# Performance work log

Measured on AMD Instinct MI355X. Metric: run time of the kernel, lower is better.

## Reference

```python
import jax, jax.numpy as jnp
import numpy as np

N_NODES = 100000
N_EDGES = 1600000
D_FEAT = 128


def setup_inputs() -> dict:
    key = jax.random.key(0)
    k1, k2, k3, k4 = jax.random.split(key, 4)
    support = jax.random.normal(k1, (N_NODES, D_FEAT), dtype=jnp.float32)
    vals = jax.random.uniform(k2, (N_EDGES,), dtype=jnp.float32)
    rows = jax.random.randint(k3, (N_EDGES,), 0, N_NODES, dtype=jnp.int64)
    cols = jax.random.randint(k4, (N_EDGES,), 0, N_NODES, dtype=jnp.int64)
    return {"support": support, "vals": vals, "rows": rows, "cols": cols}


def reference(support, vals, rows, cols):
    # out = adj @ support, adj given in COO: adj[rows[e], cols[e]] = vals[e]
    # Gather neighbor features, scale by edge weight, scatter-add to row nodes.
    msgs = vals[:, None] * support[cols]          # [E, F]
    out = jax.ops.segment_sum(msgs, rows, num_segments=support.shape[0])  # [N, F]
    return out
```

## Files before the change

### kernel.cpp

```cpp
#include <hip/hip_runtime.h>
#include <hip/hip_bf16.h>
#include <hip/hip_fp16.h>


#define D_FEAT 128
#define F4 32
#define H4 32
#define STRIDE 64
#define CELL 32
#define OVF_CAP 131072
#define EPT 8
#define MAXIT 8
#define MAXSLOT 8192

typedef float    vfloat4 __attribute__((ext_vector_type(4)));
typedef _Float16 half4v  __attribute__((ext_vector_type(4)));
typedef _Float16 half8v  __attribute__((ext_vector_type(8)));


__global__ __launch_bounds__(1024) void
phase1_bin_kernel(const float4* __restrict__ support4,
                  half8v* __restrict__ supporth,
                  const int* __restrict__ rows,
                  const int* __restrict__ cols,
                  const float* __restrict__ vals,
                  int2* __restrict__ coarse,
                  int* __restrict__ cellcnt,
                  int4* __restrict__ ovf,
                  int* __restrict__ ovf_count,
                  int E, int BT, int NBLK, int ND, int n8) {
    int b = blockIdx.x;
    int tid = threadIdx.x;

    if (b >= NBLK) {
        int m = (b - NBLK) * 1024 + tid;
        if (m < n8) {
            float4 a0 = support4[(size_t)m * 2];
            float4 a1 = support4[(size_t)m * 2 + 1];
            half8v h;
            h[0] = (_Float16)a0.x; h[1] = (_Float16)a0.y;
            h[2] = (_Float16)a0.z; h[3] = (_Float16)a0.w;
            h[4] = (_Float16)a1.x; h[5] = (_Float16)a1.y;
            h[6] = (_Float16)a1.z; h[7] = (_Float16)a1.w;
            supporth[m] = h;
        }
        return;
    }

    __shared__ int hist[512];
    for (int i = tid; i < 512; i += 1024) hist[i] = 0;
    __syncthreads();

    int t = b * 1024 + tid;
    int   r[EPT];
    int   c[EPT];
    float v[EPT];
    int   rk[EPT];

    #pragma unroll
    for (int i = 0; i < EPT; ++i) {
        int e = t + i * BT;
        r[i] = (e < E) ? rows[e] : -1;
    }
    #pragma unroll
    for (int i = 0; i < EPT; ++i) {
        int e = t + i * BT;
        if (e < E) { c[i] = cols[e]; v[i] = vals[e]; }
    }
    #pragma unroll
    for (int i = 0; i < EPT; ++i)
        rk[i] = (r[i] >= 0) ? atomicAdd(&hist[r[i] >> 8], 1) : 0;

    #pragma unroll
    for (int i = 0; i < EPT; ++i) {
        if (r[i] < 0) continue;
        int d = r[i] >> 8;
        if (rk[i] < CELL) {
            int2 q;
            q.x = ((r[i] & 255) << 17) | c[i];
            q.y = __float_as_int(v[i]);
            coarse[((size_t)d * NBLK + b) * CELL + rk[i]] = q;
        } else {
            int o = atomicAdd(ovf_count, 1);
            if (o < OVF_CAP) {
                int4 q;
                q.x = r[i]; q.y = c[i]; q.z = __float_as_int(v[i]); q.w = 0;
                ovf[o] = q;
            }
        }
    }
    __syncthreads();
    for (int d = tid; d < ND; d += 1024) {
        int h = hist[d];
        cellcnt[(size_t)d * NBLK + b] = (h < CELL) ? h : CELL;
    }
}


__global__ __launch_bounds__(1024) void
bucket_csr_gather_kernel(const half4v* __restrict__ supporth,
                         const int2* __restrict__ coarse,
                         const int* __restrict__ cellcnt,
                         float4* __restrict__ out4,
                         int NBLK, int N) {
    __shared__ int  cnt[257];
    __shared__ int  off[257];
    __shared__ int2 csr[MAXSLOT + 8];

    const int d   = blockIdx.x;
    const int tid = threadIdx.x;
    const int2* cbase = coarse  + (size_t)d * NBLK * CELL;
    const int*  ccnt  = cellcnt + (size_t)d * NBLK;
    const int total = NBLK * CELL;

    if (tid < 257) cnt[tid] = 0;
    __syncthreads();

    int2 ent[MAXIT];
    int  err[MAXIT];
    int  ernk[MAXIT];
    #pragma unroll
    for (int it = 0; it < MAXIT; ++it) {
        int s = tid + it * 1024;
        err[it] = -1;
        if (s < total && (s & (CELL - 1)) < ccnt[s >> 5]) {
            int2 q = cbase[s];
            int r = (q.x >> 17) & 255;
            ent[it].x = q.x & 0x1FFFF;
            ent[it].y = q.y;
            err[it] = r;
            ernk[it] = atomicAdd(&cnt[r], 1);
        }
    }
    __syncthreads();

    if (tid < 64) {
        int4 c4 = ((int4*)cnt)[tid];
        int t0 = c4.x;
        int t1 = t0 + c4.y;
        int t2 = t1 + c4.z;
        int t3 = t2 + c4.w;
        int inc = t3;
        #pragma unroll
        for (int dd = 1; dd < 64; dd <<= 1) {
            int t = __shfl_up(inc, dd, 64);
            if (tid >= dd) inc += t;
        }
        int excl = inc - t3;
        off[tid * 4 + 0] = excl;
        off[tid * 4 + 1] = excl + t0;
        off[tid * 4 + 2] = excl + t1;
        off[tid * 4 + 3] = excl + t2;
        if (tid == 63) off[256] = inc;
    }
    __syncthreads();

    #pragma unroll
    for (int it = 0; it < MAXIT; ++it) {
        if (err[it] >= 0)
            csr[off[err[it]] + ernk[it]] = ent[it];
    }
    __syncthreads();

    const int grp = tid >> 5;
    const int j   = tid & 31;
    const int base = d << 8;
    for (int rq = 0; rq < 8; ++rq) {
        int r   = (rq << 5) + grp;
        int beg = off[r];
        int end = off[r + 1];
        float4 acc[4];
        #pragma unroll
        for (int u = 0; u < 4; ++u) acc[u] = {0.f, 0.f, 0.f, 0.f};
        for (int k0 = beg; k0 < end; k0 += 8) {
            int   cc[8];
            float vv[8];
            #pragma unroll
            for (int u = 0; u < 8; ++u) {
                int2 e = csr[k0 + u];
                bool ib = (k0 + u) < end;
                cc[u] = ib ? e.x : 0;
                vv[u] = ib ? __int_as_float(e.y) : 0.f;
            }
            half4v s[8];
            #pragma unroll
            for (int u = 0; u < 8; ++u)
                s[u] = supporth[(size_t)cc[u] * H4 + j];
            #pragma unroll
            for (int u = 0; u < 8; ++u) {
                acc[u & 3].x += vv[u] * (float)s[u][0];
                acc[u & 3].y += vv[u] * (float)s[u][1];
                acc[u & 3].z += vv[u] * (float)s[u][2];
                acc[u & 3].w += vv[u] * (float)s[u][3];
            }
        }
        int row = base + r;
        if (row < N) {
            vfloat4 res;
            res.x = (acc[0].x + acc[1].x) + (acc[2].x + acc[3].x);
            res.y = (acc[0].y + acc[1].y) + (acc[2].y + acc[3].y);
            res.z = (acc[0].z + acc[1].z) + (acc[2].z + acc[3].z);
            res.w = (acc[0].w + acc[1].w) + (acc[2].w + acc[3].w);
            __builtin_nontemporal_store(res, (vfloat4*)&out4[(size_t)row * F4 + j]);
        }
    }
}


__global__ void ovf_scatter_kernel(const float* __restrict__ support,
                                   const int4* __restrict__ ovf,
                                   const int* __restrict__ ovf_count,
                                   float* __restrict__ out, int cap) {
    int gid = blockIdx.x * blockDim.x + threadIdx.x;
    int i = gid >> 5;
    int j = gid & 31;
    int istride = (gridDim.x * blockDim.x) >> 5;
    int cnt = *ovf_count;
    if (cnt > cap) cnt = cap;
    for (; i < cnt; i += istride) {
        int4 q = ovf[i];
        float v = __int_as_float(q.z);
        const float4* s4 = (const float4*)support + (size_t)q.y * F4 + j;
        float4 s = *s4;
        float* o = out + (size_t)q.x * D_FEAT + j * 4;
        unsafeAtomicAdd(o + 0, v * s.x);
        unsafeAtomicAdd(o + 1, v * s.y);
        unsafeAtomicAdd(o + 2, v * s.z);
        unsafeAtomicAdd(o + 3, v * s.w);
    }
}


__global__ void convert_kernel(const float4* __restrict__ in,
                               half8v* __restrict__ out, int n8) {
    int t = blockIdx.x * blockDim.x + threadIdx.x;
    if (t >= n8) return;
    float4 a = in[(size_t)t * 2];
    float4 b = in[(size_t)t * 2 + 1];
    half8v h;
    h[0] = (_Float16)a.x; h[1] = (_Float16)a.y;
    h[2] = (_Float16)a.z; h[3] = (_Float16)a.w;
    h[4] = (_Float16)b.x; h[5] = (_Float16)b.y;
    h[6] = (_Float16)b.z; h[7] = (_Float16)b.w;
    out[t] = h;
}

__global__ void gather_half_kernel(const half4v* __restrict__ supporth,
                                   const int* __restrict__ cursor,
                                   const int2* __restrict__ pairs,
                                   float4* __restrict__ out4, int n_nodes) {
    unsigned int t = blockIdx.x * blockDim.x + threadIdx.x;
    unsigned int row = t >> 5;
    unsigned int j = t & 31;
    if (row >= (unsigned int)n_nodes) return;
    int deg = cursor[row];
    if (deg > STRIDE) deg = STRIDE;
    const int2* pr = pairs + (size_t)row * STRIDE;
    int2 z = {0, 0};
    int2 p0 = ((int)j < deg) ? pr[j] : z;
    int2 p1 = ((int)(j + 32) < deg) ? pr[j + 32] : z;
    int   c0 = p0.x;  float v0 = __int_as_float(p0.y);
    int   c1 = p1.x;  float v1 = __int_as_float(p1.y);
    int degr = (deg + 7) & ~7;
    float4 acc[4];
    #pragma unroll
    for (int u = 0; u < 4; ++u) acc[u] = {0.f, 0.f, 0.f, 0.f};
    for (int k = 0; k < degr; k += 8) {
        int   cc[8];
        float vv[8];
        #pragma unroll
        for (int u = 0; u < 8; ++u) {
            int kk = k + u;
            cc[u] = __shfl(kk < 32 ? c0 : c1, kk & 31, 32);
            vv[u] = __shfl(kk < 32 ? v0 : v1, kk & 31, 32);
        }
        half4v s[8];
        #pragma unroll
        for (int u = 0; u < 8; ++u)
            s[u] = supporth[(size_t)cc[u] * H4 + j];
        #pragma unroll
        for (int u = 0; u < 8; ++u) {
            acc[u & 3].x += vv[u] * (float)s[u][0];
            acc[u & 3].y += vv[u] * (float)s[u][1];
            acc[u & 3].z += vv[u] * (float)s[u][2];
            acc[u & 3].w += vv[u] * (float)s[u][3];
        }
    }
    vfloat4 res;
    res.x = (acc[0].x + acc[1].x) + (acc[2].x + acc[3].x);
    res.y = (acc[0].y + acc[1].y) + (acc[2].y + acc[3].y);
    res.z = (acc[0].z + acc[1].z) + (acc[2].z + acc[3].z);
    res.w = (acc[0].w + acc[1].w) + (acc[2].w + acc[3].w);
    __builtin_nontemporal_store(res, (vfloat4*)&out4[(size_t)row * F4 + j]);
}

__global__ void bucket_ilp_kernel(const int* __restrict__ rows,
                                  const int* __restrict__ cols,
                                  const float* __restrict__ vals,
                                  int* __restrict__ cursor,
                                  int* __restrict__ ovf_count,
                                  int2* __restrict__ pairs,
                                  int4* __restrict__ ovf,
                                  int n_edges, int gstride) {
    int tid = blockIdx.x * blockDim.x + threadIdx.x;
    int   r[EPT];
    int   c[EPT];
    float v[EPT];
    int   slot[EPT];
    #pragma unroll
    for (int i = 0; i < EPT; ++i) {
        int e = tid + i * gstride;
        r[i] = (e < n_edges) ? rows[e] : -1;
    }
    #pragma unroll
    for (int i = 0; i < EPT; ++i) {
        int e = tid + i * gstride;
        if (e < n_edges) { c[i] = cols[e]; v[i] = vals[e]; }
    }
    #pragma unroll
    for (int i = 0; i < EPT; ++i)
        slot[i] = (r[i] >= 0) ? atomicAdd(&cursor[r[i]], 1) : 0;
    #pragma unroll
    for (int i = 0; i < EPT; ++i) {
        if (r[i] < 0) continue;
        int2 p;
        p.x = c[i];
        p.y = __float_as_int(v[i]);
        if (slot[i] < STRIDE) {
            pairs[(size_t)r[i] * STRIDE + slot[i]] = p;
        } else {
            int o = atomicAdd(ovf_count, 1);
            if (o < OVF_CAP) {
                int4 q; q.x = r[i]; q.y = p.x; q.z = p.y; q.w = 0;
                ovf[o] = q;
            }
        }
    }
}


__global__ void gc_scatter_kernel(const float* __restrict__ support,
                                  const float* __restrict__ vals,
                                  const int* __restrict__ rows,
                                  const int* __restrict__ cols,
                                  float* __restrict__ out, int n_edges) {
    unsigned int t = blockIdx.x * blockDim.x + threadIdx.x;
    unsigned int e = t >> 5;
    unsigned int j = t & 31;
    if (e >= (unsigned int)n_edges) return;
    int r = rows[e];
    int c = cols[e];
    float v = vals[e];
    const float4* s4 = reinterpret_cast<const float4*>(support) + (size_t)c * F4 + j;
    float4 s = *s4;
    float* o = out + (size_t)r * D_FEAT + j * 4;
    unsafeAtomicAdd(o + 0, v * s.x);
    unsafeAtomicAdd(o + 1, v * s.y);
    unsafeAtomicAdd(o + 2, v * s.z);
    unsafeAtomicAdd(o + 3, v * s.w);
}


extern "C" void kernel_launch(void* const* d_in, const int* in_sizes, int n_in,
                              void* d_out, int out_size, void* d_ws, size_t ws_size,
                              hipStream_t stream) {
    const float* support = (const float*)d_in[0];
    const float* vals    = (const float*)d_in[1];
    const int*   rows    = (const int*)d_in[2];
    const int*   cols    = (const int*)d_in[3];
    float* out = (float*)d_out;

    int E = in_sizes[1];
    int N = in_sizes[0] / D_FEAT;
    int n8 = N * D_FEAT / 8;
    int ND = (N + 255) >> 8;
    int NBLK = (E + 1024 * EPT - 1) / (1024 * EPT);
    int BT = NBLK * 1024;

    char* ws = (char*)d_ws;
    size_t cur = 0;
    auto carve = [&](size_t bytes) -> void* {
        void* p = ws + cur;
        cur += (bytes + 255) & ~(size_t)255;
        return p;
    };

    {
        size_t save = cur;
        int2*   coarse    = (int2*)carve((size_t)ND * NBLK * CELL * 8);
        int*    cellcnt   = (int*)carve((size_t)ND * NBLK * 4);
        int4*   ovf       = (int4*)carve((size_t)OVF_CAP * 16);
        int*    ovf_count = (int*)carve(256);
        half8v* supporth  = (half8v*)carve((size_t)N * D_FEAT * 2);
        if (cur <= ws_size && ND <= 512 && NBLK * CELL <= MAXSLOT) {
            (void)hipMemsetAsync(ovf_count, 0, 4, stream);
            int cblocks = (n8 + 1023) / 1024;
            phase1_bin_kernel<<<NBLK + cblocks, 1024, 0, stream>>>(
                (const float4*)support, supporth, rows, cols, vals,
                coarse, cellcnt, ovf, ovf_count, E, BT, NBLK, ND, n8);
            bucket_csr_gather_kernel<<<ND, 1024, 0, stream>>>(
                (const half4v*)supporth, coarse, cellcnt, (float4*)out, NBLK, N);
            ovf_scatter_kernel<<<512, 256, 0, stream>>>(
                support, ovf, ovf_count, out, OVF_CAP);
            return;
        }
        cur = save;
    }

    {
        size_t save = cur;
        int*    cursor   = (int*)carve((size_t)(N + 1) * 4);
        int2*   pairs    = (int2*)carve((size_t)N * STRIDE * 8);
        int4*   ovf      = (int4*)carve((size_t)8192 * 16);
        half8v* supporth = (half8v*)carve((size_t)N * D_FEAT * 2);
        if (cur <= ws_size) {
            int* ovf_count = cursor + N;
            int bthreads = (E + EPT - 1) / EPT;
            int bblocks = (bthreads + 255) / 256;
            int gstride = bblocks * 256;
            (void)hipMemsetAsync(cursor, 0, (size_t)(N + 1) * 4, stream);
            convert_kernel<<<(n8 + 255) / 256, 256, 0, stream>>>(
                (const float4*)support, supporth, n8);
            bucket_ilp_kernel<<<bblocks, 256, 0, stream>>>(
                rows, cols, vals, cursor, ovf_count, pairs, ovf, E, gstride);
            unsigned int gthreads = (unsigned int)N * 32;
            gather_half_kernel<<<(gthreads + 255) / 256, 256, 0, stream>>>(
                (const half4v*)supporth, cursor, pairs, (float4*)out, N);
            ovf_scatter_kernel<<<512, 256, 0, stream>>>(
                support, ovf, ovf_count, out, 8192);
            return;
        }
        cur = save;
    }

    (void)hipMemsetAsync(d_out, 0, (size_t)out_size * sizeof(float), stream);
    unsigned int total = (unsigned int)E * 32;
    gc_scatter_kernel<<<(total + 255) / 256, 256, 0, stream>>>(
        support, vals, rows, cols, out, E);
}
```

Before: 202.2 us.

## Use 16-byte half8 gathers in bucket kernel and split conversion into separate kernel

In the gather phase, 16 lanes per row each load a half8 vector of 16 bytes instead of 32 lanes loading half4, so one row's feature vector takes fewer, wider load instructions, and each block now handles 64 rows per pass instead of 32. Each thread keeps two split accumulators of eight floats and issues two float4 stores. The fp32-to-fp16 conversion of support is moved out of the binning kernel into its own launch of 256-thread blocks. That adds a kernel launch and serializes conversion after binning, where the two previously ran together in one grid.

New measurement: 211.2 us. 1.04x slower.

```diff
diff --git a/kernel.cpp b/kernel.cpp
--- a/kernel.cpp
+++ b/kernel.cpp
@@ -6,6 +6,7 @@
 #define D_FEAT 128
 #define F4 32
 #define H4 32
+#define H8 16
 #define STRIDE 64
 #define CELL 32
 #define OVF_CAP 131072
@@ -19,33 +20,16 @@
 
 
 __global__ __launch_bounds__(1024) void
-phase1_bin_kernel(const float4* __restrict__ support4,
-                  half8v* __restrict__ supporth,
-                  const int* __restrict__ rows,
-                  const int* __restrict__ cols,
-                  const float* __restrict__ vals,
-                  int2* __restrict__ coarse,
-                  int* __restrict__ cellcnt,
-                  int4* __restrict__ ovf,
-                  int* __restrict__ ovf_count,
-                  int E, int BT, int NBLK, int ND, int n8) {
+bin_kernel(const int* __restrict__ rows,
+           const int* __restrict__ cols,
+           const float* __restrict__ vals,
+           int2* __restrict__ coarse,
+           int* __restrict__ cellcnt,
+           int4* __restrict__ ovf,
+           int* __restrict__ ovf_count,
+           int E, int BT, int NBLK, int ND) {
     int b = blockIdx.x;
     int tid = threadIdx.x;
-
-    if (b >= NBLK) {
-        int m = (b - NBLK) * 1024 + tid;
-        if (m < n8) {
-            float4 a0 = support4[(size_t)m * 2];
-            float4 a1 = support4[(size_t)m * 2 + 1];
-            half8v h;
-            h[0] = (_Float16)a0.x; h[1] = (_Float16)a0.y;
-            h[2] = (_Float16)a0.z; h[3] = (_Float16)a0.w;
-            h[4] = (_Float16)a1.x; h[5] = (_Float16)a1.y;
-            h[6] = (_Float16)a1.z; h[7] = (_Float16)a1.w;
-            supporth[m] = h;
-        }
-        return;
-    }
 
     __shared__ int hist[512];
     for (int i = tid; i < 512; i += 1024) hist[i] = 0;
@@ -97,8 +81,23 @@
 }
 
 
+__global__ void convert_kernel(const float4* __restrict__ in,
+                               half8v* __restrict__ out, int n8) {
+    int t = blockIdx.x * blockDim.x + threadIdx.x;
+    if (t >= n8) return;
+    float4 a = in[(size_t)t * 2];
+    float4 b = in[(size_t)t * 2 + 1];
+    half8v h;
+    h[0] = (_Float16)a.x; h[1] = (_Float16)a.y;
+    h[2] = (_Float16)a.z; h[3] = (_Float16)a.w;
+    h[4] = (_Float16)b.x; h[5] = (_Float16)b.y;
+    h[6] = (_Float16)b.z; h[7] = (_Float16)b.w;
+    out[t] = h;
+}
+
+
 __global__ __launch_bounds__(1024) void
-bucket_csr_gather_kernel(const half4v* __restrict__ supporth,
+bucket_csr_gather_kernel(const half8v* __restrict__ supporth,
                          const int2* __restrict__ coarse,
                          const int* __restrict__ cellcnt,
                          float4* __restrict__ out4,
@@ -162,16 +161,15 @@
     }
     __syncthreads();
 
-    const int grp = tid >> 5;
-    const int j   = tid & 31;
+    const int g = tid >> 4;
+    const int i = tid & 15;
     const int base = d << 8;
-    for (int rq = 0; rq < 8; ++rq) {
-        int r   = (rq << 5) + grp;
+    for (int rq = 0; rq < 4; ++rq) {
+        int r   = (rq << 6) + g;
         int beg = off[r];
         int end = off[r + 1];
-        float4 acc[4];
-        #pragma unroll
-        for (int u = 0; u < 4; ++u) acc[u] = {0.f, 0.f, 0.f, 0.f};
+        vfloat4 a00 = {0.f,0.f,0.f,0.f}, a01 = {0.f,0.f,0.f,0.f};
+        vfloat4 a10 = {0.f,0.f,0.f,0.f}, a11 = {0.f,0.f,0.f,0.f};
         for (int k0 = beg; k0 < end; k0 += 8) {
             int   cc[8];
             float vv[8];
@@ -182,26 +180,44 @@
                 cc[u] = ib ? e.x : 0;
                 vv[u] = ib ? __int_as_float(e.y) : 0.f;
             }
-            half4v s[8];
+            half8v s[8];
             #pragma unroll
             for (int u = 0; u < 8; ++u)
-                s[u] = supporth[(size_t)cc[u] * H4 + j];
+                s[u] = supporth[(size_t)cc[u] * H8 + i];
             #pragma unroll
             for (int u = 0; u < 8; ++u) {
-                acc[u & 3].x += vv[u] * (float)s[u][0];
-                acc[u & 3].y += vv[u] * (float)s[u][1];
-                acc[u & 3].z += vv[u] * (float)s[u][2];
-                acc[u & 3].w += vv[u] * (float)s[u][3];
+                float v = vv[u];
+                if (u & 1) {
+                    a10.x += v * (float)s[u][0];
+                    a10.y += v * (float)s[u][1];
+                    a10.z += v * (float)s[u][2];
+                    a10.w += v * (float)s[u][3];
+                    a11.x += v * (float)s[u][4];
+                    a11.y += v * (float)s[u][5];
+                    a11.z += v * (float)s[u][6];
+                    a11.w += v * (float)s[u][7];
+                } else {
+                    a00.x += v * (float)s[u][0];
+                    a00.y += v * (float)s[u][1];
+                    a00.z += v * (float)s[u][2];
+                    a00.w += v * (float)s[u][3];
+                    a01.x += v * (float)s[u][4];
+                    a01.y += v * (float)s[u][5];
+                    a01.z += v * (float)s[u][6];
+                    a01.w += v * (float)s[u][7];
+                }
             }
         }
         int row = base + r;
         if (row < N) {
-            vfloat4 res;
-            res.x = (acc[0].x + acc[1].x) + (acc[2].x + acc[3].x);
-            res.y = (acc[0].y + acc[1].y) + (acc[2].y + acc[3].y);
-            res.z = (acc[0].z + acc[1].z) + (acc[2].z + acc[3].z);
-            res.w = (acc[0].w + acc[1].w) + (acc[2].w + acc[3].w);
-            __builtin_nontemporal_store(res, (vfloat4*)&out4[(size_t)row * F4 + j]);
+            vfloat4 r0, r1;
+            r0.x = a00.x + a10.x; r0.y = a00.y + a10.y;
+            r0.z = a00.z + a10.z; r0.w = a00.w + a10.w;
+            r1.x = a01.x + a11.x; r1.y = a01.y + a11.y;
+            r1.z = a01.z + a11.z; r1.w = a01.w + a11.w;
+            float4* dst = &out4[(size_t)row * F4 + (i << 1)];
+            __builtin_nontemporal_store(r0, (vfloat4*)dst);
+            __builtin_nontemporal_store(r1, (vfloat4*)(dst + 1));
         }
     }
 }
@@ -231,20 +247,6 @@
 }
 
 
-__global__ void convert_kernel(const float4* __restrict__ in,
-                               half8v* __restrict__ out, int n8) {
-    int t = blockIdx.x * blockDim.x + threadIdx.x;
-    if (t >= n8) return;
-    float4 a = in[(size_t)t * 2];
-    float4 b = in[(size_t)t * 2 + 1];
-    half8v h;
-    h[0] = (_Float16)a.x; h[1] = (_Float16)a.y;
-    h[2] = (_Float16)a.z; h[3] = (_Float16)a.w;
-    h[4] = (_Float16)b.x; h[5] = (_Float16)b.y;
-    h[6] = (_Float16)b.z; h[7] = (_Float16)b.w;
-    out[t] = h;
-}
-
 __global__ void gather_half_kernel(const half4v* __restrict__ supporth,
                                    const int* __restrict__ cursor,
                                    const int2* __restrict__ pairs,
@@ -394,12 +396,13 @@
         half8v* supporth  = (half8v*)carve((size_t)N * D_FEAT * 2);
         if (cur <= ws_size && ND <= 512 && NBLK * CELL <= MAXSLOT) {
             (void)hipMemsetAsync(ovf_count, 0, 4, stream);
-            int cblocks = (n8 + 1023) / 1024;
-            phase1_bin_kernel<<<NBLK + cblocks, 1024, 0, stream>>>(
-                (const float4*)support, supporth, rows, cols, vals,
-                coarse, cellcnt, ovf, ovf_count, E, BT, NBLK, ND, n8);
+            bin_kernel<<<NBLK, 1024, 0, stream>>>(
+                rows, cols, vals, coarse, cellcnt, ovf, ovf_count,
+                E, BT, NBLK, ND);
+            convert_kernel<<<(n8 + 255) / 256, 256, 0, stream>>>(
+                (const float4*)support, supporth, n8);
             bucket_csr_gather_kernel<<<ND, 1024, 0, stream>>>(
-                (const half4v*)supporth, coarse, cellcnt, (float4*)out, NBLK, N);
+                supporth, coarse, cellcnt, (float4*)out, NBLK, N);
             ovf_scatter_kernel<<<512, 256, 0, stream>>>(
                 support, ovf, ovf_count, out, OVF_CAP);
             return;
```
